# Kernel optimization log

Measured on AMD Instinct MI355X. Metric: run time of the kernel, lower is better.

The kernel has to match this reference:

```python
import jax, jax.numpy as jnp
import numpy as np

H, W = 256, 832            # full-res organized point cloud (HEIGHT/WIDTH globals)
STRIDE_H, STRIDE_W = 2, 4  # stride_H_list[0], stride_W_list[0]
OUT_H, OUT_W = 128, 208    # out_H_list[0], out_W_list[0]
KH, KW = 12, 20            # layer0 kernel_size
K = 32                     # layer0 K_sample


def _sa_layer(pts, h_idx, w_idx, w1, b1, w2, b2, w3, b3):
    """PointNet SA: strided center selection, window KNN grouping, MLP, max-pool.
    pts: (B,H,W,3); h_idx/w_idx: (M,) full-res grid coords of selected centers.
    """
    B = pts.shape[0]
    pts_flat = pts.reshape(B, H * W, 3)
    center_idx = h_idx * W + w_idx                      # (M,)
    centers = pts_flat[:, center_idx]                   # (B,M,3)  fast_select gather
    # candidate window around each center (clipped at borders)
    dh = jnp.arange(KH) - KH // 2
    dw = jnp.arange(KW) - KW // 2
    cand_h = jnp.clip(h_idx[:, None] + dh, 0, H - 1)    # (M,KH)
    cand_w = jnp.clip(w_idx[:, None] + dw, 0, W - 1)    # (M,KW)
    cand_idx = (cand_h[:, :, None] * W + cand_w[:, None, :]).reshape(-1, KH * KW)  # (M,P)
    cand = pts_flat[:, cand_idx]                        # (B,M,P,3) irregular gather
    d2 = jnp.sum((cand - centers[:, :, None, :]) ** 2, axis=-1)  # (B,M,P)
    _, nn = jax.lax.top_k(-d2, K)                       # K nearest within window
    knn = jnp.take_along_axis(cand, nn[..., None], axis=2)       # (B,M,K,3)
    rel = knn - centers[:, :, None, :]                  # local coordinates
    h = jax.nn.relu(rel @ w1 + b1)                      # mlp [8,8,16]
    h = jax.nn.relu(h @ w2 + b2)
    h = jax.nn.relu(h @ w3 + b3)
    return centers, jnp.max(h, axis=2)                  # (B,M,3), (B,M,16)


def setup_inputs() -> dict:
    key = jax.random.key(0)
    ks = jax.random.split(key, 5)
    return {
        "pos1": jax.random.normal(ks[0], (2, H, W, 3), jnp.float32) * 5.0,
        "pos2": jax.random.normal(ks[1], (2, H, W, 3), jnp.float32) * 5.0,
        "w1": jax.random.normal(ks[2], (3, 8), jnp.float32) * 0.3,
        "b1": jnp.zeros((8,), jnp.float32),
        "w2": jax.random.normal(ks[3], (8, 8), jnp.float32) * 0.3,
        "b2": jnp.zeros((8,), jnp.float32),
        "w3": jax.random.normal(ks[4], (8, 16), jnp.float32) * 0.3,
        "b3": jnp.zeros((16,), jnp.float32),
    }


def reference(pos1, pos2, w1, b1, w2, b2, w3, b3):
    # get_selected_idx for level 0: strided grid subsampling
    h_idx = jnp.repeat(jnp.arange(OUT_H) * STRIDE_H, OUT_W)  # (M,)
    w_idx = jnp.tile(jnp.arange(OUT_W) * STRIDE_W, OUT_H)    # (M,)
    _, f1 = _sa_layer(pos1, h_idx, w_idx, w1, b1, w2, b2, w3, b3)
    _, f2 = _sa_layer(pos2, h_idx, w_idx, w1, b1, w2, b2, w3, b3)
    return jnp.concatenate([f1, f2], axis=-1)  # (B, OUT_H*OUT_W, 32)
```

## Files before the change

kernel.cpp:

```cpp
#include <hip/hip_runtime.h>
#include <hip/hip_bf16.h>

#define HH 256
#define WW 832
#define OHH 128
#define OWW 208
#define NCAND 240
#define MM (OHH*OWW)

typedef float v2f __attribute__((ext_vector_type(2)));

__device__ __forceinline__ int iclamp(int v, int lo, int hi) { return min(max(v, lo), hi); }
__device__ __forceinline__ int mbcnt2(unsigned long long m) {
    return __builtin_amdgcn_mbcnt_hi((unsigned)(m >> 32),
           __builtin_amdgcn_mbcnt_lo((unsigned)m, 0));
}
__device__ __forceinline__ v2f sxor(v2f v, int m) {
    v2f r; r.x = __shfl_xor(v.x, m); r.y = __shfl_xor(v.y, m); return r;
}
__device__ __forceinline__ v2f lo2(float4 f) { return (v2f){f.x, f.y}; }
__device__ __forceinline__ v2f hi2(float4 f) { return (v2f){f.z, f.w}; }

__global__ void __launch_bounds__(256) sa_fused(
    const float* __restrict__ pos1, const float* __restrict__ pos2,
    const float* __restrict__ w1, const float* __restrict__ b1,
    const float* __restrict__ w2, const float* __restrict__ b2,
    const float* __restrict__ w3, const float* __restrict__ b3,
    float* __restrict__ out)
{
    __shared__ float4 sW1q[3][2];
    __shared__ float4 sW2q[8][2];
    __shared__ float4 sW3q[8][4];
    __shared__ float4 sB1q[2], sB2q[2], sB3q[4];
    __shared__ float4 selRel[256];

    const int t = threadIdx.x;
    if (t < 6)            { int i = t >> 1, qd = (t & 1) * 4;
        sW1q[i][t & 1] = make_float4(w1[i*8+qd], w1[i*8+qd+1], w1[i*8+qd+2], w1[i*8+qd+3]); }
    if (t >= 8 && t < 24) { int u = t - 8, i = u >> 1, qd = (u & 1) * 4;
        sW2q[i][u & 1] = make_float4(w2[i*8+qd], w2[i*8+qd+1], w2[i*8+qd+2], w2[i*8+qd+3]); }
    if (t >= 32 && t < 64){ int u = t - 32, i = u >> 2, qd = (u & 3) * 4;
        sW3q[i][u & 3] = make_float4(w3[i*16+qd], w3[i*16+qd+1], w3[i*16+qd+2], w3[i*16+qd+3]); }
    if (t >= 64 && t < 66){ int u = (t - 64) * 4; sB1q[t-64] = make_float4(b1[u], b1[u+1], b1[u+2], b1[u+3]); }
    if (t >= 66 && t < 68){ int u = (t - 66) * 4; sB2q[t-66] = make_float4(b2[u], b2[u+1], b2[u+2], b2[u+3]); }
    if (t >= 68 && t < 72){ int u = (t - 68) * 4; sB3q[t-68] = make_float4(b3[u], b3[u+1], b3[u+2], b3[u+3]); }
    __syncthreads();

    const int lane = t & 63;
    const int wid  = t >> 6;
    const int l31  = lane & 31;
    const int mA   = blockIdx.x * 8 + wid * 2;
    const int b    = blockIdx.y & 1;
    const int cl   = blockIdx.y >> 1;
    const float* __restrict__ base = (cl ? pos2 : pos1) + (size_t)b * (HH * WW * 3);

    int kh  = (lane * 3277) >> 14;
    int kwb = (lane - kh * 5) * 4;
    if (lane >= 60) { kh = 11; kwb = 0; }

    #pragma unroll
    for (int cc = 0; cc < 2; ++cc) {
        const int m  = mA + cc;
        const int oh = (int)(((unsigned)(m >> 4) * 5042u) >> 16);
        const int ow = m - oh * OWW;
        const int h0 = oh * 2, w0 = ow * 4;

        const float cx = base[(h0 * WW + w0) * 3 + 0];
        const float cy = base[(h0 * WW + w0) * 3 + 1];
        const float cz = base[(h0 * WW + w0) * 3 + 2];

        unsigned d2b[4];
        float rxv[4], ryv[4], rzv[4];
        const bool interior = ((unsigned)(oh - 3) <= 122u) && ((unsigned)(ow - 3) <= 202u);
        if (interior) {
            const float* p = base + ((h0 - 6 + kh) * WW + (w0 - 10 + kwb)) * 3;
            float2 Av = *(const float2*)(p);
            float4 Bv = *(const float4*)(p + 2);
            float4 Cv = *(const float4*)(p + 6);
            float2 Dv = *(const float2*)(p + 10);
            float px[4] = {Av.x, Bv.y, Cv.x, Cv.w};
            float py[4] = {Av.y, Bv.z, Cv.y, Dv.x};
            float pz[4] = {Bv.x, Bv.w, Cv.z, Dv.y};
            #pragma unroll
            for (int q = 0; q < 4; ++q) {
                float dx = __fsub_rn(px[q], cx);
                float dy = __fsub_rn(py[q], cy);
                float dz = __fsub_rn(pz[q], cz);
                rxv[q] = dx; ryv[q] = dy; rzv[q] = dz;
                d2b[q] = __float_as_uint(__fadd_rn(__fadd_rn(__fmul_rn(dx, dx), __fmul_rn(dy, dy)), __fmul_rn(dz, dz)));
            }
        } else {
            int chh = iclamp(h0 - 6 + kh, 0, HH - 1);
            #pragma unroll
            for (int q = 0; q < 4; ++q) {
                int cw = iclamp(w0 - 10 + kwb + q, 0, WW - 1);
                const float* p = base + (chh * WW + cw) * 3;
                float dx = __fsub_rn(p[0], cx);
                float dy = __fsub_rn(p[1], cy);
                float dz = __fsub_rn(p[2], cz);
                rxv[q] = dx; ryv[q] = dy; rzv[q] = dz;
                d2b[q] = __float_as_uint(__fadd_rn(__fadd_rn(__fmul_rn(dx, dx), __fmul_rn(dy, dy)), __fmul_rn(dz, dz)));
            }
        }
        if (lane >= 60) { d2b[0] = d2b[1] = d2b[2] = d2b[3] = 0xFFFFFFFFu; }

        unsigned T = 0; int c0 = 0; bool exact = false;
        unsigned long long sv0 = 0, sv1 = 0, sv2 = 0, sv3 = 0;
        for (int bpos = 30; bpos >= 0; --bpos) {
            unsigned Q = T | (1u << bpos);
            unsigned long long t0 = __ballot(d2b[0] < Q);
            unsigned long long t1 = __ballot(d2b[1] < Q);
            unsigned long long t2 = __ballot(d2b[2] < Q);
            unsigned long long t3 = __ballot(d2b[3] < Q);
            int c = __popcll(t0) + __popcll(t1) + __popcll(t2) + __popcll(t3);
            if (c == 32) { T = Q; exact = true; sv0 = t0; sv1 = t1; sv2 = t2; sv3 = t3; break; }
            if (c < 32)  { T = Q; c0 = c; }
        }

        bool m0, m1, m2, m3;
        unsigned long long s0, s1, s2, s3;
        if (exact) {
            m0 = (d2b[0] < T); m1 = (d2b[1] < T); m2 = (d2b[2] < T); m3 = (d2b[3] < T);
            s0 = sv0; s1 = sv1; s2 = sv2; s3 = sv3;
        } else {
            const int r = 32 - c0;
            bool eq0 = (d2b[0] == T), eq1 = (d2b[1] == T), eq2 = (d2b[2] == T), eq3 = (d2b[3] == T);
            unsigned long long e0 = __ballot(eq0);
            unsigned long long e1 = __ballot(eq1);
            unsigned long long e2 = __ballot(eq2);
            unsigned long long e3 = __ballot(eq3);
            int SA = mbcnt2(e0) + mbcnt2(e1) + mbcnt2(e2) + mbcnt2(e3);
            int E1 = (int)eq0, E2 = E1 + (int)eq1, E3 = E2 + (int)eq2;
            m0 = (d2b[0] < T) || (eq0 && (SA      < r));
            m1 = (d2b[1] < T) || (eq1 && (SA + E1 < r));
            m2 = (d2b[2] < T) || (eq2 && (SA + E2 < r));
            m3 = (d2b[3] < T) || (eq3 && (SA + E3 < r));
            s0 = __ballot(m0); s1 = __ballot(m1); s2 = __ballot(m2); s3 = __ballot(m3);
        }

        {
            int p1 = __popcll(s0);
            int p2 = p1 + __popcll(s1);
            int p3 = p2 + __popcll(s2);
            int lb = wid * 64 + cc * 32;
            if (m0) selRel[lb +      mbcnt2(s0)] = make_float4(rxv[0], ryv[0], rzv[0], 0.f);
            if (m1) selRel[lb + p1 + mbcnt2(s1)] = make_float4(rxv[1], ryv[1], rzv[1], 0.f);
            if (m2) selRel[lb + p2 + mbcnt2(s2)] = make_float4(rxv[2], ryv[2], rzv[2], 0.f);
            if (m3) selRel[lb + p3 + mbcnt2(s3)] = make_float4(rxv[3], ryv[3], rzv[3], 0.f);
        }
    }
    asm volatile("s_waitcnt lgkmcnt(0)" ::: "memory");
    __builtin_amdgcn_sched_barrier(0);

    {
        float4 rel = selRel[wid * 64 + lane];
        v2f rx2 = (v2f){rel.x, rel.x};
        v2f ry2 = (v2f){rel.y, rel.y};
        v2f rz2 = (v2f){rel.z, rel.z};

        v2f a1[4];
        {
            float4 bq0 = sB1q[0], bq1 = sB1q[1];
            float4 x0 = sW1q[0][0], x1 = sW1q[0][1];
            float4 y0 = sW1q[1][0], y1 = sW1q[1][1];
            float4 z0 = sW1q[2][0], z1 = sW1q[2][1];
            a1[0] = __builtin_elementwise_fma(rx2, lo2(x0), lo2(bq0));
            a1[1] = __builtin_elementwise_fma(rx2, hi2(x0), hi2(bq0));
            a1[2] = __builtin_elementwise_fma(rx2, lo2(x1), lo2(bq1));
            a1[3] = __builtin_elementwise_fma(rx2, hi2(x1), hi2(bq1));
            a1[0] = __builtin_elementwise_fma(ry2, lo2(y0), a1[0]);
            a1[1] = __builtin_elementwise_fma(ry2, hi2(y0), a1[1]);
            a1[2] = __builtin_elementwise_fma(ry2, lo2(y1), a1[2]);
            a1[3] = __builtin_elementwise_fma(ry2, hi2(y1), a1[3]);
            a1[0] = __builtin_elementwise_fma(rz2, lo2(z0), a1[0]);
            a1[1] = __builtin_elementwise_fma(rz2, hi2(z0), a1[1]);
            a1[2] = __builtin_elementwise_fma(rz2, lo2(z1), a1[2]);
            a1[3] = __builtin_elementwise_fma(rz2, hi2(z1), a1[3]);
            #pragma unroll
            for (int op = 0; op < 4; ++op) a1[op] = __builtin_elementwise_max(a1[op], (v2f)(0.f));
        }
        v2f a2[4] = {lo2(sB2q[0]), hi2(sB2q[0]), lo2(sB2q[1]), hi2(sB2q[1])};
        #pragma unroll
        for (int i = 0; i < 8; ++i) {
            float h = a1[i >> 1][i & 1];
            v2f hb = (v2f){h, h};
            float4 wl = sW2q[i][0], wh = sW2q[i][1];
            a2[0] = __builtin_elementwise_fma(hb, lo2(wl), a2[0]);
            a2[1] = __builtin_elementwise_fma(hb, hi2(wl), a2[1]);
            a2[2] = __builtin_elementwise_fma(hb, lo2(wh), a2[2]);
            a2[3] = __builtin_elementwise_fma(hb, hi2(wh), a2[3]);
        }
        #pragma unroll
        for (int op = 0; op < 4; ++op) a2[op] = __builtin_elementwise_max(a2[op], (v2f)(0.f));

        v2f a3[8] = {lo2(sB3q[0]), hi2(sB3q[0]), lo2(sB3q[1]), hi2(sB3q[1]),
                     lo2(sB3q[2]), hi2(sB3q[2]), lo2(sB3q[3]), hi2(sB3q[3])};
        #pragma unroll
        for (int i = 0; i < 8; ++i) {
            float h = a2[i >> 1][i & 1];
            v2f hb = (v2f){h, h};
            float4 q0 = sW3q[i][0], q1 = sW3q[i][1], q2 = sW3q[i][2], q3 = sW3q[i][3];
            a3[0] = __builtin_elementwise_fma(hb, lo2(q0), a3[0]);
            a3[1] = __builtin_elementwise_fma(hb, hi2(q0), a3[1]);
            a3[2] = __builtin_elementwise_fma(hb, lo2(q1), a3[2]);
            a3[3] = __builtin_elementwise_fma(hb, hi2(q1), a3[3]);
            a3[4] = __builtin_elementwise_fma(hb, lo2(q2), a3[4]);
            a3[5] = __builtin_elementwise_fma(hb, hi2(q2), a3[5]);
            a3[6] = __builtin_elementwise_fma(hb, lo2(q3), a3[6]);
            a3[7] = __builtin_elementwise_fma(hb, hi2(q3), a3[7]);
        }

        #pragma unroll
        for (int step = 16; step >= 1; step >>= 1) {
            #pragma unroll
            for (int op = 0; op < 8; ++op)
                a3[op] = __builtin_elementwise_max(a3[op], sxor(a3[op], step));
        }
        if (l31 == 0) {
            #pragma unroll
            for (int op = 0; op < 8; ++op)
                a3[op] = __builtin_elementwise_max(a3[op], (v2f)(0.f));
            const int ms = mA + (lane >> 5);
            float4* dst = (float4*)(out + ((size_t)(b * MM + ms) * 32) + (size_t)cl * 16);
            dst[0] = make_float4(a3[0].x, a3[0].y, a3[1].x, a3[1].y);
            dst[1] = make_float4(a3[2].x, a3[2].y, a3[3].x, a3[3].y);
            dst[2] = make_float4(a3[4].x, a3[4].y, a3[5].x, a3[5].y);
            dst[3] = make_float4(a3[6].x, a3[6].y, a3[7].x, a3[7].y);
        }
    }
}

extern "C" void kernel_launch(void* const* d_in, const int* in_sizes, int n_in,
                              void* d_out, int out_size, void* d_ws, size_t ws_size,
                              hipStream_t stream) {
    const float* pos1 = (const float*)d_in[0];
    const float* pos2 = (const float*)d_in[1];
    const float* w1   = (const float*)d_in[2];
    const float* b1   = (const float*)d_in[3];
    const float* w2   = (const float*)d_in[4];
    const float* b2   = (const float*)d_in[5];
    const float* w3   = (const float*)d_in[6];
    const float* b3   = (const float*)d_in[7];
    float* out = (float*)d_out;

    dim3 grid(MM / 8, 4);
    sa_fused<<<grid, 256, 0, stream>>>(pos1, pos2, w1, b1, w2, b2, w3, b3, out);
}
```

Before: 88.45 us.

## Interleave two centers' radix selects and store indices instead of relative coords

```diff
diff --git a/kernel.cpp b/kernel.cpp
--- a/kernel.cpp
+++ b/kernel.cpp
@@ -9,9 +9,10 @@
 #define MM (OHH*OWW)
 
 typedef float v2f __attribute__((ext_vector_type(2)));
+typedef unsigned long long ull;
 
 __device__ __forceinline__ int iclamp(int v, int lo, int hi) { return min(max(v, lo), hi); }
-__device__ __forceinline__ int mbcnt2(unsigned long long m) {
+__device__ __forceinline__ int mbcnt2(ull m) {
     return __builtin_amdgcn_mbcnt_hi((unsigned)(m >> 32),
            __builtin_amdgcn_mbcnt_lo((unsigned)m, 0));
 }
@@ -32,7 +33,7 @@
     __shared__ float4 sW2q[8][2];
     __shared__ float4 sW3q[8][4];
     __shared__ float4 sB1q[2], sB2q[2], sB3q[4];
-    __shared__ float4 selRel[256];
+    __shared__ int selJ[256];
 
     const int t = threadIdx.x;
     if (t < 6)            { int i = t >> 1, qd = (t & 1) * 4;
@@ -49,6 +50,7 @@
     const int lane = t & 63;
     const int wid  = t >> 6;
     const int l31  = lane & 31;
+    const int half = lane >> 5;
     const int mA   = blockIdx.x * 8 + wid * 2;
     const int b    = blockIdx.y & 1;
     const int cl   = blockIdx.y >> 1;
@@ -58,19 +60,21 @@
     int kwb = (lane - kh * 5) * 4;
     if (lane >= 60) { kh = 11; kwb = 0; }
 
-    #pragma unroll
-    for (int cc = 0; cc < 2; ++cc) {
-        const int m  = mA + cc;
+    unsigned dA0, dA1, dA2, dA3, dB0, dB1, dB2, dB3;
+    int h0A, w0A, h0B, w0B;
+    float cxA, cyA, czA, cxB, cyB, czB;
+
+    auto distpass = [&](int m, unsigned& D0, unsigned& D1, unsigned& D2, unsigned& D3,
+                        int& h0o, int& w0o, float& cxo, float& cyo, float& czo) {
         const int oh = (int)(((unsigned)(m >> 4) * 5042u) >> 16);
         const int ow = m - oh * OWW;
         const int h0 = oh * 2, w0 = ow * 4;
-
+        h0o = h0; w0o = w0;
         const float cx = base[(h0 * WW + w0) * 3 + 0];
         const float cy = base[(h0 * WW + w0) * 3 + 1];
         const float cz = base[(h0 * WW + w0) * 3 + 2];
-
+        cxo = cx; cyo = cy; czo = cz;
         unsigned d2b[4];
-        float rxv[4], ryv[4], rzv[4];
         const bool interior = ((unsigned)(oh - 3) <= 122u) && ((unsigned)(ow - 3) <= 202u);
         if (interior) {
             const float* p = base + ((h0 - 6 + kh) * WW + (w0 - 10 + kwb)) * 3;
@@ -86,7 +90,6 @@
                 float dx = __fsub_rn(px[q], cx);
                 float dy = __fsub_rn(py[q], cy);
                 float dz = __fsub_rn(pz[q], cz);
-                rxv[q] = dx; ryv[q] = dy; rzv[q] = dz;
                 d2b[q] = __float_as_uint(__fadd_rn(__fadd_rn(__fmul_rn(dx, dx), __fmul_rn(dy, dy)), __fmul_rn(dz, dz)));
             }
         } else {
@@ -98,65 +101,112 @@
                 float dx = __fsub_rn(p[0], cx);
                 float dy = __fsub_rn(p[1], cy);
                 float dz = __fsub_rn(p[2], cz);
-                rxv[q] = dx; ryv[q] = dy; rzv[q] = dz;
                 d2b[q] = __float_as_uint(__fadd_rn(__fadd_rn(__fmul_rn(dx, dx), __fmul_rn(dy, dy)), __fmul_rn(dz, dz)));
             }
         }
         if (lane >= 60) { d2b[0] = d2b[1] = d2b[2] = d2b[3] = 0xFFFFFFFFu; }
-
-        unsigned T = 0; int c0 = 0; bool exact = false;
-        unsigned long long sv0 = 0, sv1 = 0, sv2 = 0, sv3 = 0;
-        for (int bpos = 30; bpos >= 0; --bpos) {
-            unsigned Q = T | (1u << bpos);
-            unsigned long long t0 = __ballot(d2b[0] < Q);
-            unsigned long long t1 = __ballot(d2b[1] < Q);
-            unsigned long long t2 = __ballot(d2b[2] < Q);
-            unsigned long long t3 = __ballot(d2b[3] < Q);
+        D0 = d2b[0]; D1 = d2b[1]; D2 = d2b[2]; D3 = d2b[3];
+    };
+    distpass(mA,     dA0, dA1, dA2, dA3, h0A, w0A, cxA, cyA, czA);
+    distpass(mA + 1, dB0, dB1, dB2, dB3, h0B, w0B, cxB, cyB, czB);
+
+    unsigned TA = 0, TB = 0; int c0A = 0, c0B = 0;
+    bool exactA = false, exactB = false;
+    ull svA0 = 0, svA1 = 0, svA2 = 0, svA3 = 0;
+    ull svB0 = 0, svB1 = 0, svB2 = 0, svB3 = 0;
+    for (int bpos = 30; bpos >= 0; --bpos) {
+        if (!exactA) {
+            unsigned Q = TA | (1u << bpos);
+            ull t0 = __ballot(dA0 < Q);
+            ull t1 = __ballot(dA1 < Q);
+            ull t2 = __ballot(dA2 < Q);
+            ull t3 = __ballot(dA3 < Q);
             int c = __popcll(t0) + __popcll(t1) + __popcll(t2) + __popcll(t3);
-            if (c == 32) { T = Q; exact = true; sv0 = t0; sv1 = t1; sv2 = t2; sv3 = t3; break; }
-            if (c < 32)  { T = Q; c0 = c; }
-        }
-
-        bool m0, m1, m2, m3;
-        unsigned long long s0, s1, s2, s3;
-        if (exact) {
-            m0 = (d2b[0] < T); m1 = (d2b[1] < T); m2 = (d2b[2] < T); m3 = (d2b[3] < T);
-            s0 = sv0; s1 = sv1; s2 = sv2; s3 = sv3;
+            if (c == 32) { TA = Q; exactA = true; svA0 = t0; svA1 = t1; svA2 = t2; svA3 = t3; }
+            else if (c < 32) { TA = Q; c0A = c; }
+        }
+        if (!exactB) {
+            unsigned Q = TB | (1u << bpos);
+            ull t0 = __ballot(dB0 < Q);
+            ull t1 = __ballot(dB1 < Q);
+            ull t2 = __ballot(dB2 < Q);
+            ull t3 = __ballot(dB3 < Q);
+            int c = __popcll(t0) + __popcll(t1) + __popcll(t2) + __popcll(t3);
+            if (c == 32) { TB = Q; exactB = true; svB0 = t0; svB1 = t1; svB2 = t2; svB3 = t3; }
+            else if (c < 32) { TB = Q; c0B = c; }
+        }
+        if (exactA && exactB) break;
+    }
+
+    {
+        bool m0, m1, m2, m3; ull s0, s1, s2, s3;
+        if (exactA) {
+            m0 = (dA0 < TA); m1 = (dA1 < TA); m2 = (dA2 < TA); m3 = (dA3 < TA);
+            s0 = svA0; s1 = svA1; s2 = svA2; s3 = svA3;
         } else {
-            const int r = 32 - c0;
-            bool eq0 = (d2b[0] == T), eq1 = (d2b[1] == T), eq2 = (d2b[2] == T), eq3 = (d2b[3] == T);
-            unsigned long long e0 = __ballot(eq0);
-            unsigned long long e1 = __ballot(eq1);
-            unsigned long long e2 = __ballot(eq2);
-            unsigned long long e3 = __ballot(eq3);
+            const int r = 32 - c0A;
+            bool eq0 = (dA0 == TA), eq1 = (dA1 == TA), eq2 = (dA2 == TA), eq3 = (dA3 == TA);
+            ull e0 = __ballot(eq0), e1 = __ballot(eq1), e2 = __ballot(eq2), e3 = __ballot(eq3);
             int SA = mbcnt2(e0) + mbcnt2(e1) + mbcnt2(e2) + mbcnt2(e3);
             int E1 = (int)eq0, E2 = E1 + (int)eq1, E3 = E2 + (int)eq2;
-            m0 = (d2b[0] < T) || (eq0 && (SA      < r));
-            m1 = (d2b[1] < T) || (eq1 && (SA + E1 < r));
-            m2 = (d2b[2] < T) || (eq2 && (SA + E2 < r));
-            m3 = (d2b[3] < T) || (eq3 && (SA + E3 < r));
+            m0 = (dA0 < TA) || (eq0 && (SA      < r));
+            m1 = (dA1 < TA) || (eq1 && (SA + E1 < r));
+            m2 = (dA2 < TA) || (eq2 && (SA + E2 < r));
+            m3 = (dA3 < TA) || (eq3 && (SA + E3 < r));
             s0 = __ballot(m0); s1 = __ballot(m1); s2 = __ballot(m2); s3 = __ballot(m3);
         }
-
-        {
-            int p1 = __popcll(s0);
-            int p2 = p1 + __popcll(s1);
-            int p3 = p2 + __popcll(s2);
-            int lb = wid * 64 + cc * 32;
-            if (m0) selRel[lb +      mbcnt2(s0)] = make_float4(rxv[0], ryv[0], rzv[0], 0.f);
-            if (m1) selRel[lb + p1 + mbcnt2(s1)] = make_float4(rxv[1], ryv[1], rzv[1], 0.f);
-            if (m2) selRel[lb + p2 + mbcnt2(s2)] = make_float4(rxv[2], ryv[2], rzv[2], 0.f);
-            if (m3) selRel[lb + p3 + mbcnt2(s3)] = make_float4(rxv[3], ryv[3], rzv[3], 0.f);
-        }
+        int p1 = __popcll(s0), p2 = p1 + __popcll(s1), p3 = p2 + __popcll(s2);
+        int lb = wid * 64;
+        int j4 = lane * 4;
+        if (m0) selJ[lb +      mbcnt2(s0)] = j4;
+        if (m1) selJ[lb + p1 + mbcnt2(s1)] = j4 + 1;
+        if (m2) selJ[lb + p2 + mbcnt2(s2)] = j4 + 2;
+        if (m3) selJ[lb + p3 + mbcnt2(s3)] = j4 + 3;
+    }
+    {
+        bool m0, m1, m2, m3; ull s0, s1, s2, s3;
+        if (exactB) {
+            m0 = (dB0 < TB); m1 = (dB1 < TB); m2 = (dB2 < TB); m3 = (dB3 < TB);
+            s0 = svB0; s1 = svB1; s2 = svB2; s3 = svB3;
+        } else {
+            const int r = 32 - c0B;
+            bool eq0 = (dB0 == TB), eq1 = (dB1 == TB), eq2 = (dB2 == TB), eq3 = (dB3 == TB);
+            ull e0 = __ballot(eq0), e1 = __ballot(eq1), e2 = __ballot(eq2), e3 = __ballot(eq3);
+            int SA = mbcnt2(e0) + mbcnt2(e1) + mbcnt2(e2) + mbcnt2(e3);
+            int E1 = (int)eq0, E2 = E1 + (int)eq1, E3 = E2 + (int)eq2;
+            m0 = (dB0 < TB) || (eq0 && (SA      < r));
+            m1 = (dB1 < TB) || (eq1 && (SA + E1 < r));
+            m2 = (dB2 < TB) || (eq2 && (SA + E2 < r));
+            m3 = (dB3 < TB) || (eq3 && (SA + E3 < r));
+            s0 = __ballot(m0); s1 = __ballot(m1); s2 = __ballot(m2); s3 = __ballot(m3);
+        }
+        int p1 = __popcll(s0), p2 = p1 + __popcll(s1), p3 = p2 + __popcll(s2);
+        int lb = wid * 64 + 32;
+        int j4 = lane * 4;
+        if (m0) selJ[lb +      mbcnt2(s0)] = j4;
+        if (m1) selJ[lb + p1 + mbcnt2(s1)] = j4 + 1;
+        if (m2) selJ[lb + p2 + mbcnt2(s2)] = j4 + 2;
+        if (m3) selJ[lb + p3 + mbcnt2(s3)] = j4 + 3;
     }
     asm volatile("s_waitcnt lgkmcnt(0)" ::: "memory");
     __builtin_amdgcn_sched_barrier(0);
 
     {
-        float4 rel = selRel[wid * 64 + lane];
-        v2f rx2 = (v2f){rel.x, rel.x};
-        v2f ry2 = (v2f){rel.y, rel.y};
-        v2f rz2 = (v2f){rel.z, rel.z};
+        int jj = selJ[wid * 64 + lane];
+        int L  = jj >> 2, q = jj & 3;
+        int kh2 = (L * 3277) >> 14;
+        int kw2 = (L - kh2 * 5) * 4 + q;
+        int h0s = half ? h0B : h0A;
+        int w0s = half ? w0B : w0A;
+        int ch = iclamp(h0s - 6 + kh2, 0, HH - 1);
+        int cw = iclamp(w0s - 10 + kw2, 0, WW - 1);
+        const float* p = base + (ch * WW + cw) * 3;
+        float rx = __fsub_rn(p[0], half ? cxB : cxA);
+        float ry = __fsub_rn(p[1], half ? cyB : cyA);
+        float rz = __fsub_rn(p[2], half ? czB : czA);
+        v2f rx2 = (v2f){rx, rx};
+        v2f ry2 = (v2f){ry, ry};
+        v2f rz2 = (v2f){rz, rz};
 
         v2f a1[4];
         {
@@ -220,7 +270,7 @@
             #pragma unroll
             for (int op = 0; op < 8; ++op)
                 a3[op] = __builtin_elementwise_max(a3[op], (v2f)(0.f));
-            const int ms = mA + (lane >> 5);
+            const int ms = mA + half;
             float4* dst = (float4*)(out + ((size_t)(b * MM + ms) * 32) + (size_t)cl * 16);
             dst[0] = make_float4(a3[0].x, a3[0].y, a3[1].x, a3[1].y);
             dst[1] = make_float4(a3[2].x, a3[2].y, a3[3].x, a3[3].y);
```

Measured after the change: 88.91 us. No clear change (+0.5%).

## Process four centers per wave and use DPP row reductions for max-pool

Applied to the files above, without the earlier changes.

```diff
diff --git a/kernel.cpp b/kernel.cpp
--- a/kernel.cpp
+++ b/kernel.cpp
@@ -9,17 +9,30 @@
 #define MM (OHH*OWW)
 
 typedef float v2f __attribute__((ext_vector_type(2)));
+typedef unsigned long long ull;
 
 __device__ __forceinline__ int iclamp(int v, int lo, int hi) { return min(max(v, lo), hi); }
-__device__ __forceinline__ int mbcnt2(unsigned long long m) {
+__device__ __forceinline__ int mbcnt2(ull m) {
     return __builtin_amdgcn_mbcnt_hi((unsigned)(m >> 32),
            __builtin_amdgcn_mbcnt_lo((unsigned)m, 0));
 }
-__device__ __forceinline__ v2f sxor(v2f v, int m) {
-    v2f r; r.x = __shfl_xor(v.x, m); r.y = __shfl_xor(v.y, m); return r;
-}
 __device__ __forceinline__ v2f lo2(float4 f) { return (v2f){f.x, f.y}; }
 __device__ __forceinline__ v2f hi2(float4 f) { return (v2f){f.z, f.w}; }
+
+template<int CTRL>
+__device__ __forceinline__ float dppmax(float v) {
+    int r = __builtin_amdgcn_update_dpp(__float_as_int(v), __float_as_int(v),
+                                        CTRL, 0xF, 0xF, false);
+    return fmaxf(v, __int_as_float(r));
+}
+__device__ __forceinline__ float halfmax32(float v) {
+    v = dppmax<0x111>(v);
+    v = dppmax<0x112>(v);
+    v = dppmax<0x114>(v);
+    v = dppmax<0x118>(v);
+    v = dppmax<0x142>(v);
+    return v;
+}
 
 __global__ void __launch_bounds__(256) sa_fused(
     const float* __restrict__ pos1, const float* __restrict__ pos2,
@@ -32,7 +45,7 @@
     __shared__ float4 sW2q[8][2];
     __shared__ float4 sW3q[8][4];
     __shared__ float4 sB1q[2], sB2q[2], sB3q[4];
-    __shared__ float4 selRel[256];
+    __shared__ float4 selRel[512];
 
     const int t = threadIdx.x;
     if (t < 6)            { int i = t >> 1, qd = (t & 1) * 4;
@@ -49,29 +62,31 @@
     const int lane = t & 63;
     const int wid  = t >> 6;
     const int l31  = lane & 31;
-    const int mA   = blockIdx.x * 8 + wid * 2;
+    const int half = lane >> 5;
+    const int mA   = blockIdx.x * 16 + wid * 4;
     const int b    = blockIdx.y & 1;
     const int cl   = blockIdx.y >> 1;
     const float* __restrict__ base = (cl ? pos2 : pos1) + (size_t)b * (HH * WW * 3);
 
+    const int oh  = (int)(((unsigned)(mA >> 4) * 5042u) >> 16);
+    const int ow0 = mA - oh * OWW;
+    const int h0  = oh * 2;
+    const bool rowInt = ((unsigned)(oh - 3) <= 122u);
+
     int kh  = (lane * 3277) >> 14;
     int kwb = (lane - kh * 5) * 4;
     if (lane >= 60) { kh = 11; kwb = 0; }
 
-    #pragma unroll
-    for (int cc = 0; cc < 2; ++cc) {
-        const int m  = mA + cc;
-        const int oh = (int)(((unsigned)(m >> 4) * 5042u) >> 16);
-        const int ow = m - oh * OWW;
-        const int h0 = oh * 2, w0 = ow * 4;
-
-        const float cx = base[(h0 * WW + w0) * 3 + 0];
-        const float cy = base[(h0 * WW + w0) * 3 + 1];
-        const float cz = base[(h0 * WW + w0) * 3 + 2];
+    #pragma unroll 1
+    for (int cc = 0; cc < 4; ++cc) {
+        const int ow = ow0 + cc;
+        const int w0 = ow * 4;
+        const float* cp = base + (h0 * WW + w0) * 3;
+        const float cx = cp[0], cy = cp[1], cz = cp[2];
 
         unsigned d2b[4];
         float rxv[4], ryv[4], rzv[4];
-        const bool interior = ((unsigned)(oh - 3) <= 122u) && ((unsigned)(ow - 3) <= 202u);
+        const bool interior = rowInt && ((unsigned)(ow - 3) <= 202u);
         if (interior) {
             const float* p = base + ((h0 - 6 + kh) * WW + (w0 - 10 + kwb)) * 3;
             float2 Av = *(const float2*)(p);
@@ -104,56 +119,47 @@
         }
         if (lane >= 60) { d2b[0] = d2b[1] = d2b[2] = d2b[3] = 0xFFFFFFFFu; }
 
-        unsigned T = 0; int c0 = 0; bool exact = false;
-        unsigned long long sv0 = 0, sv1 = 0, sv2 = 0, sv3 = 0;
+        unsigned T = 0; int c0 = 0;
         for (int bpos = 30; bpos >= 0; --bpos) {
             unsigned Q = T | (1u << bpos);
-            unsigned long long t0 = __ballot(d2b[0] < Q);
-            unsigned long long t1 = __ballot(d2b[1] < Q);
-            unsigned long long t2 = __ballot(d2b[2] < Q);
-            unsigned long long t3 = __ballot(d2b[3] < Q);
+            ull t0 = __ballot(d2b[0] < Q);
+            ull t1 = __ballot(d2b[1] < Q);
+            ull t2 = __ballot(d2b[2] < Q);
+            ull t3 = __ballot(d2b[3] < Q);
             int c = __popcll(t0) + __popcll(t1) + __popcll(t2) + __popcll(t3);
-            if (c == 32) { T = Q; exact = true; sv0 = t0; sv1 = t1; sv2 = t2; sv3 = t3; break; }
+            if (c == 32) { T = Q; c0 = 32; break; }
             if (c < 32)  { T = Q; c0 = c; }
         }
 
         bool m0, m1, m2, m3;
-        unsigned long long s0, s1, s2, s3;
-        if (exact) {
+        if (c0 == 32) {
             m0 = (d2b[0] < T); m1 = (d2b[1] < T); m2 = (d2b[2] < T); m3 = (d2b[3] < T);
-            s0 = sv0; s1 = sv1; s2 = sv2; s3 = sv3;
         } else {
             const int r = 32 - c0;
             bool eq0 = (d2b[0] == T), eq1 = (d2b[1] == T), eq2 = (d2b[2] == T), eq3 = (d2b[3] == T);
-            unsigned long long e0 = __ballot(eq0);
-            unsigned long long e1 = __ballot(eq1);
-            unsigned long long e2 = __ballot(eq2);
-            unsigned long long e3 = __ballot(eq3);
+            ull e0 = __ballot(eq0), e1 = __ballot(eq1), e2 = __ballot(eq2), e3 = __ballot(eq3);
             int SA = mbcnt2(e0) + mbcnt2(e1) + mbcnt2(e2) + mbcnt2(e3);
             int E1 = (int)eq0, E2 = E1 + (int)eq1, E3 = E2 + (int)eq2;
             m0 = (d2b[0] < T) || (eq0 && (SA      < r));
             m1 = (d2b[1] < T) || (eq1 && (SA + E1 < r));
             m2 = (d2b[2] < T) || (eq2 && (SA + E2 < r));
             m3 = (d2b[3] < T) || (eq3 && (SA + E3 < r));
-            s0 = __ballot(m0); s1 = __ballot(m1); s2 = __ballot(m2); s3 = __ballot(m3);
-        }
-
-        {
-            int p1 = __popcll(s0);
-            int p2 = p1 + __popcll(s1);
-            int p3 = p2 + __popcll(s2);
-            int lb = wid * 64 + cc * 32;
-            if (m0) selRel[lb +      mbcnt2(s0)] = make_float4(rxv[0], ryv[0], rzv[0], 0.f);
-            if (m1) selRel[lb + p1 + mbcnt2(s1)] = make_float4(rxv[1], ryv[1], rzv[1], 0.f);
-            if (m2) selRel[lb + p2 + mbcnt2(s2)] = make_float4(rxv[2], ryv[2], rzv[2], 0.f);
-            if (m3) selRel[lb + p3 + mbcnt2(s3)] = make_float4(rxv[3], ryv[3], rzv[3], 0.f);
-        }
+        }
+
+        ull s0 = __ballot(m0), s1 = __ballot(m1), s2 = __ballot(m2), s3 = __ballot(m3);
+        int p1 = __popcll(s0), p2 = p1 + __popcll(s1), p3 = p2 + __popcll(s2);
+        float4* lb = &selRel[wid * 128 + cc * 32];
+        if (m0) lb[      mbcnt2(s0)] = make_float4(rxv[0], ryv[0], rzv[0], 0.f);
+        if (m1) lb[p1 + mbcnt2(s1)] = make_float4(rxv[1], ryv[1], rzv[1], 0.f);
+        if (m2) lb[p2 + mbcnt2(s2)] = make_float4(rxv[2], ryv[2], rzv[2], 0.f);
+        if (m3) lb[p3 + mbcnt2(s3)] = make_float4(rxv[3], ryv[3], rzv[3], 0.f);
     }
     asm volatile("s_waitcnt lgkmcnt(0)" ::: "memory");
     __builtin_amdgcn_sched_barrier(0);
 
-    {
-        float4 rel = selRel[wid * 64 + lane];
+    #pragma unroll 1
+    for (int p = 0; p < 2; ++p) {
+        float4 rel = selRel[wid * 128 + (p * 2 + half) * 32 + l31];
         v2f rx2 = (v2f){rel.x, rel.x};
         v2f ry2 = (v2f){rel.y, rel.y};
         v2f rz2 = (v2f){rel.z, rel.z};
@@ -210,22 +216,20 @@
             a3[7] = __builtin_elementwise_fma(hb, hi2(q3), a3[7]);
         }
 
-        #pragma unroll
-        for (int step = 16; step >= 1; step >>= 1) {
-            #pragma unroll
-            for (int op = 0; op < 8; ++op)
-                a3[op] = __builtin_elementwise_max(a3[op], sxor(a3[op], step));
-        }
-        if (l31 == 0) {
-            #pragma unroll
-            for (int op = 0; op < 8; ++op)
-                a3[op] = __builtin_elementwise_max(a3[op], (v2f)(0.f));
-            const int ms = mA + (lane >> 5);
+        float hv[16];
+        #pragma unroll
+        for (int op = 0; op < 8; ++op) { hv[2*op] = a3[op].x; hv[2*op+1] = a3[op].y; }
+        #pragma unroll
+        for (int o = 0; o < 16; ++o) hv[o] = halfmax32(hv[o]);
+        if (l31 == 31) {
+            #pragma unroll
+            for (int o = 0; o < 16; ++o) hv[o] = fmaxf(hv[o], 0.f);
+            const int ms = mA + p * 2 + half;
             float4* dst = (float4*)(out + ((size_t)(b * MM + ms) * 32) + (size_t)cl * 16);
-            dst[0] = make_float4(a3[0].x, a3[0].y, a3[1].x, a3[1].y);
-            dst[1] = make_float4(a3[2].x, a3[2].y, a3[3].x, a3[3].y);
-            dst[2] = make_float4(a3[4].x, a3[4].y, a3[5].x, a3[5].y);
-            dst[3] = make_float4(a3[6].x, a3[6].y, a3[7].x, a3[7].y);
+            dst[0] = make_float4(hv[0],  hv[1],  hv[2],  hv[3]);
+            dst[1] = make_float4(hv[4],  hv[5],  hv[6],  hv[7]);
+            dst[2] = make_float4(hv[8],  hv[9],  hv[10], hv[11]);
+            dst[3] = make_float4(hv[12], hv[13], hv[14], hv[15]);
         }
     }
 }
@@ -243,6 +247,6 @@
     const float* b3   = (const float*)d_in[7];
     float* out = (float*)d_out;
 
-    dim3 grid(MM / 8, 4);
+    dim3 grid(MM / 16, 4);
     sa_fused<<<grid, 256, 0, stream>>>(pos1, pos2, w1, b1, w2, b2, w3, b3, out);
 }
```

New measurement: 257.5 us. +191.1%, slower.
